# Kernel tuning notes

Hardware: AMD Instinct MI355X
Metric: run time of the kernel (lower is better)

## Reference

```python
import jax, jax.numpy as jnp
import numpy as np
import math

# static config
NH, HD, HID = 16, 128, 2048
ROT = 64            # head_dim * partial_rotary_factor(0.5)
EPS = 1e-6
GROUPS = 8
CHUNK = 64
THETA = 10000.0
LAYER_IDX, N_LAYERS = 1, 32
B, S = 2, 2048


def _base_slopes(n):
    # power-of-two branch of HF ALiBi slopes
    start = 2 ** (-(2 ** (-(math.log2(n) - 3))))
    return [start * (start ** i) for i in range(n)]

# per-head log-decay (negative): slope = -base * (1 - (l-1)/(L-1) + 1e-5)
SLOPE = jnp.asarray(
    -np.array(_base_slopes(NH), dtype=np.float32)
    * (1.0 - (LAYER_IDX - 1) / (N_LAYERS - 1) + 1e-5),
    dtype=jnp.float32)  # [NH]


def _rmsnorm(x, w):
    return x * jax.lax.rsqrt(jnp.mean(x * x, axis=-1, keepdims=True) + EPS) * w


def _partial_rope(x, positions):
    # x: [B,S,NH,HD]; neox-style rotary on first ROT dims, rest passthrough
    half = ROT // 2
    inv_freq = 1.0 / (THETA ** (jnp.arange(half, dtype=jnp.float32) / half))
    ang = positions.astype(jnp.float32)[:, None] * inv_freq       # [S, half]
    cos = jnp.cos(ang)[None, :, None, :]
    sin = jnp.sin(ang)[None, :, None, :]
    x1, x2, rest = x[..., :half], x[..., half:ROT], x[..., ROT:]
    return jnp.concatenate(
        [x1 * cos - x2 * sin, x2 * cos + x1 * sin, rest], axis=-1)


def setup_inputs() -> dict:
    key = jax.random.key(0)
    ks = jax.random.split(key, 4)
    return {
        'positions': jnp.arange(S, dtype=jnp.int32),
        'hidden_states': jax.random.normal(ks[0], (B, S, HID), jnp.float32),
        'recurrent_state': jnp.zeros((B, NH, HD, HD), jnp.float32),
        'w_qkv': jax.random.normal(ks[1], (HID, 3 * NH * HD), jnp.float32) * 0.02,
        'w_g': jax.random.normal(ks[2], (HID, NH * HD), jnp.float32) * 0.02,
        'w_dense': jax.random.normal(ks[3], (NH * HD, HID), jnp.float32) * 0.02,
        'q_norm_w': jnp.ones((HD,), jnp.float32),
        'k_norm_w': jnp.ones((HD,), jnp.float32),
        'g_norm_w': jnp.ones((NH * HD,), jnp.float32),
    }


def reference(positions, hidden_states, recurrent_state, w_qkv, w_g, w_dense,
              q_norm_w, k_norm_w, g_norm_w):
    # fused QKV projection
    qkv = hidden_states @ w_qkv                       # [B,S,3*NH*HD]
    q, k, v = jnp.split(qkv, 3, axis=-1)
    q = q.reshape(B, S, NH, HD)
    k = k.reshape(B, S, NH, HD)
    v = v.reshape(B, S, NH, HD)

    # QK RMSNorm then partial rotary
    q = _partial_rope(_rmsnorm(q, q_norm_w), positions)
    k = _partial_rope(_rmsnorm(k, k_norm_w), positions)

    # chunked ALiBi-decayed linear attention:
    #   S_t = lam * S_{t-1} + k_t v_t^T ; o_t = q_t S_t, lam = exp(slope)
    NC = S // CHUNK
    qc = q.reshape(B, NC, CHUNK, NH, HD).transpose(1, 0, 3, 2, 4)  # [NC,B,NH,C,HD]
    kc = k.reshape(B, NC, CHUNK, NH, HD).transpose(1, 0, 3, 2, 4)
    vc = v.reshape(B, NC, CHUNK, NH, HD).transpose(1, 0, 3, 2, 4)

    t = jnp.arange(CHUNK, dtype=jnp.float32)
    # intra-chunk causal decay mask lam^(i-j), i>=j: [NH,C,C]
    dec_mask = jnp.where(t[:, None] >= t[None, :],
                         jnp.exp(SLOPE[:, None, None] * (t[:, None] - t[None, :])),
                         0.0)
    q_dec = jnp.exp(SLOPE[:, None] * (t[None, :] + 1.0))            # [NH,C] lam^(i+1)
    k_dec = jnp.exp(SLOPE[:, None] * (CHUNK - 1.0 - t[None, :]))    # [NH,C] lam^(C-1-j)
    lam_C = jnp.exp(SLOPE * CHUNK)                                   # [NH]

    def step(state, inp):
        qb, kb, vb = inp                                  # [B,NH,C,HD]
        scores = jnp.einsum('bhid,bhjd->bhij', qb, kb) * dec_mask[None]
        o_intra = jnp.einsum('bhij,bhjd->bhid', scores, vb)
        o_inter = jnp.einsum('bhid,bhde->bhie', qb * q_dec[None, :, :, None], state)
        new_state = (state * lam_C[None, :, None, None]
                     + jnp.einsum('bhjd,bhje->bhde', kb * k_dec[None, :, :, None], vb))
        return new_state, o_intra + o_inter

    _, o = jax.lax.scan(step, recurrent_state, (qc, kc, vc))  # o: [NC,B,NH,C,HD]
    o = o.transpose(1, 0, 3, 2, 4).reshape(B, S, NH * HD)

    # GroupRMSNorm on attention output, sigmoid gate, output projection
    og = o.reshape(B, S, GROUPS, (NH * HD) // GROUPS)
    og = og * jax.lax.rsqrt(jnp.mean(og * og, axis=-1, keepdims=True) + EPS)
    o = og.reshape(B, S, NH * HD) * g_norm_w
    o = o * jax.nn.sigmoid(hidden_states @ w_g)
    return o @ w_dense
```

## Files before the change

kernel.cpp:

```cpp
#include <hip/hip_runtime.h>
#include <hip/hip_bf16.h>
#include <math.h>

#define NH   16
#define HD   128
#define HID  2048
#define NKV  6144
#define B_   2
#define S_   2048
#define NC   32
#define CHUNK_ 64
#define GROUPS_ 8

typedef __bf16 bf16_t;
typedef bf16_t bf16x8 __attribute__((ext_vector_type(8)));
typedef float  f32x4  __attribute__((ext_vector_type(4)));

__device__ __forceinline__ float b2f(unsigned int u) {
    union { unsigned int u; float f; } c; c.u = (u & 0xffffu) << 16; return c.f;
}
__device__ __forceinline__ unsigned int f2b(float f) {
    union { float f; unsigned int u; } c; c.f = f;
    unsigned int u = c.u;
    return (u + 0x7fffu + ((u >> 16) & 1u)) >> 16;
}

#define GLOAD_LDS16(gp, lp) __builtin_amdgcn_global_load_lds(                     \
    (const __attribute__((address_space(1))) void*)(gp),                          \
    (__attribute__((address_space(3))) void*)(lp), 16, 0, 0)

__global__ __launch_bounds__(256) void cvt_bf16(const float* __restrict__ in,
                                                unsigned short* __restrict__ out, int n8)
{
    int i = blockIdx.x * 256 + threadIdx.x;
    if (i >= n8) return;
    const float4* p = (const float4*)in + (size_t)i * 2;
    float4 a = p[0], b = p[1];
    uint4 o;
    o.x = f2b(a.x) | (f2b(a.y) << 16);
    o.y = f2b(a.z) | (f2b(a.w) << 16);
    o.z = f2b(b.x) | (f2b(b.y) << 16);
    o.w = f2b(b.z) | (f2b(b.w) << 16);
    ((uint4*)out)[i] = o;
}

__global__ __launch_bounds__(256) void transpose_cvt(const float* __restrict__ in,
                                                     unsigned short* __restrict__ out,
                                                     int Kdim, int Ndim)
{
    __shared__ float tile[32][33];
    int ntx = Ndim >> 5;
    int bx = blockIdx.x % ntx;
    int by = blockIdx.x / ntx;
    int lx = threadIdx.x & 31, ly = threadIdx.x >> 5;
    int r0 = by * 32, c0 = bx * 32;
    #pragma unroll
    for (int r = 0; r < 4; ++r)
        tile[ly + r * 8][lx] = in[(size_t)(r0 + ly + r * 8) * Ndim + c0 + lx];
    __syncthreads();
    #pragma unroll
    for (int r = 0; r < 4; ++r)
        out[(size_t)(c0 + ly + r * 8) * Kdim + r0 + lx] = (unsigned short)f2b(tile[lx][ly + r * 8]);
}

__device__ __forceinline__ void storeOne(float* p, float v) { *p = v; }
__device__ __forceinline__ void storeOne(unsigned short* p, float v) { *p = (unsigned short)f2b(v); }

template <typename OutT>
__global__ __launch_bounds__(256) void gemm_mfma(const bf16_t* __restrict__ A,
                                                 const bf16_t* __restrict__ Bt,
                                                 OutT* __restrict__ C,
                                                 int M, int N, int K)
{
    __shared__ bf16_t As[128 * 32];
    __shared__ bf16_t Bs[128 * 32];
    int tid  = threadIdx.x;
    int ntiles = N >> 7;
    int bx = blockIdx.x % ntiles;
    int by = blockIdx.x / ntiles;
    int lane = tid & 63;
    int wave = tid >> 6;
    int wm = (wave >> 1) * 64;
    int wn = (wave & 1) * 64;
    int l16  = lane & 15;
    int quad = lane >> 4;

    f32x4 acc[4][4];
    #pragma unroll
    for (int i = 0; i < 4; ++i)
        #pragma unroll
        for (int j = 0; j < 4; ++j) { f32x4 z = {0.f, 0.f, 0.f, 0.f}; acc[i][j] = z; }

    const bf16_t* aG = A  + (size_t)(by * 128 + (tid >> 2)) * K + (tid & 3) * 8;
    const bf16_t* bG = Bt + (size_t)(bx * 128 + (tid >> 2)) * K + (tid & 3) * 8;
    bf16_t* aL0 = As + tid * 8;
    bf16_t* aL1 = As + 2048 + tid * 8;
    bf16_t* bL0 = Bs + tid * 8;
    bf16_t* bL1 = Bs + 2048 + tid * 8;
    const size_t half = (size_t)64 * K;

    for (int kt = 0; kt < K; kt += 32) {
        GLOAD_LDS16(aG + kt,        aL0);
        GLOAD_LDS16(aG + half + kt, aL1);
        GLOAD_LDS16(bG + kt,        bL0);
        GLOAD_LDS16(bG + half + kt, bL1);
        __syncthreads();
        bf16x8 af[4], bf[4];
        #pragma unroll
        for (int t = 0; t < 4; ++t) {
            af[t] = *(const bf16x8*)(As + (wm + t * 16 + l16) * 32 + quad * 8);
            bf[t] = *(const bf16x8*)(Bs + (wn + t * 16 + l16) * 32 + quad * 8);
        }
        #pragma unroll
        for (int mt = 0; mt < 4; ++mt)
            #pragma unroll
            for (int nt = 0; nt < 4; ++nt)
                acc[mt][nt] = __builtin_amdgcn_mfma_f32_16x16x32_bf16(af[mt], bf[nt], acc[mt][nt], 0, 0, 0);
        __syncthreads();
    }

    #pragma unroll
    for (int mt = 0; mt < 4; ++mt)
        #pragma unroll
        for (int nt = 0; nt < 4; ++nt) {
            int col = bx * 128 + wn + nt * 16 + l16;
            #pragma unroll
            for (int r = 0; r < 4; ++r) {
                int row = by * 128 + wm + mt * 16 + quad * 4 + r;
                storeOne(C + (size_t)row * N + col, acc[mt][nt][r]);
            }
        }
}


__device__ __forceinline__ void ld_fr4(bf16x8 (&d)[4][2], const bf16_t* b, int s0, int ri) {
    #pragma unroll
    for (int i = 0; i < 4; ++i)
        #pragma unroll
        for (int k = 0; k < 2; ++k)
            d[i][k] = *(const bf16x8*)(b + (((s0 + i) * 2 + k) << 9) + ri);
}
__device__ __forceinline__ void ld_fr2(bf16x8 (&d)[2][2], const bf16_t* b, int s0, int ri) {
    #pragma unroll
    for (int i = 0; i < 2; ++i)
        #pragma unroll
        for (int k = 0; k < 2; ++k)
            d[i][k] = *(const bf16x8*)(b + (((s0 + i) * 2 + k) << 9) + ri);
}
__device__ __forceinline__ void mfma_quad(f32x4 (&a)[4][2], const bf16x8 (&af)[4][2],
                                          const bf16x8 (&bv)[2][2]) {
    #pragma unroll
    for (int mt = 0; mt < 4; ++mt)
        #pragma unroll
        for (int nt = 0; nt < 2; ++nt)
            #pragma unroll
            for (int ks = 0; ks < 2; ++ks)
                a[mt][nt] = __builtin_amdgcn_mfma_f32_16x16x32_bf16(af[mt][ks], bv[nt][ks], a[mt][nt], 0, 0, 0);
}

#define BAR()     asm volatile("s_barrier" ::: "memory")
#define VMCNT0()  asm volatile("s_waitcnt vmcnt(0)" ::: "memory")

__global__ __launch_bounds__(512, 2) void gemm_qg_256(const bf16_t* __restrict__ A,
                                                      const bf16_t* __restrict__ Bt,
                                                      unsigned short* __restrict__ Cq,
                                                      unsigned short* __restrict__ Cg)
{
    __shared__ bf16_t Asm[2][2][8192];
    __shared__ bf16_t Bsm[2][2][8192];
    const int K  = HID;
    const int NT = K / 64;

    int tid  = threadIdx.x;
    int wave = tid >> 6, lane = tid & 63;
    int wm = wave >> 2, wn = wave & 3;
    int l16 = lane & 15, quad = lane >> 4;
    int wm4 = wm * 4, wn2 = wn * 2;

    int bid = blockIdx.x;
    int xcd = bid & 7, idx = bid >> 3;
    int by  = (xcd >> 2) * 8 + (idx >> 3);
    int bx  = (xcd & 3) * 8 + (idx & 7);

    int rd_in = ((l16 << 5) | (quad << 3)) ^ (((l16 >> 3) & 1) << 4);

    int ch = lane ^ ((lane & 32) >> 4);
    int rr = ch >> 2;
    int cc = (ch & 3) * 8;

    const bf16_t* aSrc0 = A  + (size_t)(by * 256 +       wave * 16 + rr) * K + cc;
    const bf16_t* aSrc1 = A  + (size_t)(by * 256 + 128 + wave * 16 + rr) * K + cc;
    const bf16_t* bSrc0 = Bt + (size_t)(bx * 256 +       wave * 16 + rr) * K + cc;
    const bf16_t* bSrc1 = Bt + (size_t)(bx * 256 + 128 + wave * 16 + rr) * K + cc;

#define STAGE_A(h, t) do {                                                        \
        const bf16_t* _g = ((h) ? aSrc1 : aSrc0) + (size_t)(t) * 64;              \
        bf16_t* _l = &Asm[(t) & 1][(h)][wave * 1024 + lane * 8];                  \
        GLOAD_LDS16(_g,      _l);                                                 \
        GLOAD_LDS16(_g + 32, _l + 512); } while (0)
#define STAGE_B(h, t) do {                                                        \
        const bf16_t* _g = ((h) ? bSrc1 : bSrc0) + (size_t)(t) * 64;              \
        bf16_t* _l = &Bsm[(t) & 1][(h)][wave * 1024 + lane * 8];                  \
        GLOAD_LDS16(_g,      _l);                                                 \
        GLOAD_LDS16(_g + 32, _l + 512); } while (0)

    f32x4 acc[2][2][4][2];
    #pragma unroll
    for (int a0 = 0; a0 < 2; ++a0)
        #pragma unroll
        for (int a1 = 0; a1 < 2; ++a1)
            #pragma unroll
            for (int a2 = 0; a2 < 4; ++a2)
                #pragma unroll
                for (int a3 = 0; a3 < 2; ++a3) { f32x4 z = {0.f,0.f,0.f,0.f}; acc[a0][a1][a2][a3] = z; }

    STAGE_A(0, 0); STAGE_B(0, 0); STAGE_A(1, 0); STAGE_B(1, 0);
    VMCNT0();
    BAR();

    #pragma unroll 2
    for (int t = 0; t < NT - 1; ++t) {
        const int buf = t & 1;
        STAGE_A(0, t + 1); STAGE_B(0, t + 1); STAGE_A(1, t + 1); STAGE_B(1, t + 1);
        {
            bf16x8 afA[4][2], afB[4][2], bf0[2][2], bf1[2][2];
            ld_fr4(afA, &Asm[buf][0][0], wm4, rd_in);
            ld_fr2(bf0, &Bsm[buf][0][0], wn2, rd_in);
            mfma_quad(acc[0][0], afA, bf0);
            ld_fr2(bf1, &Bsm[buf][1][0], wn2, rd_in);
            mfma_quad(acc[0][1], afA, bf1);
            ld_fr4(afB, &Asm[buf][1][0], wm4, rd_in);
            mfma_quad(acc[1][1], afB, bf1);
            mfma_quad(acc[1][0], afB, bf0);
        }
        VMCNT0();
        BAR();
    }
    {
        const int buf = (NT - 1) & 1;
        bf16x8 afA[4][2], afB[4][2], bf0[2][2], bf1[2][2];
        ld_fr4(afA, &Asm[buf][0][0], wm4, rd_in);
        ld_fr2(bf0, &Bsm[buf][0][0], wn2, rd_in);
        mfma_quad(acc[0][0], afA, bf0);
        ld_fr2(bf1, &Bsm[buf][1][0], wn2, rd_in);
        mfma_quad(acc[0][1], afA, bf1);
        ld_fr4(afB, &Asm[buf][1][0], wm4, rd_in);
        mfma_quad(acc[1][1], afB, bf1);
        mfma_quad(acc[1][0], afB, bf0);
    }
#undef STAGE_A
#undef STAGE_B

    unsigned short* Cc; int Nn, colbase;
    if (bx < 24) { Cc = Cq; Nn = NKV; colbase = bx * 256; }
    else         { Cc = Cg; Nn = HID; colbase = bx * 256 - NKV; }
    int row0 = by * 256 + wm * 64 + quad * 4;
    int col0 = colbase + wn * 32 + l16;
    #pragma unroll
    for (int mh = 0; mh < 2; ++mh)
        #pragma unroll
        for (int nh = 0; nh < 2; ++nh)
            #pragma unroll
            for (int mt = 0; mt < 4; ++mt)
                #pragma unroll
                for (int nt = 0; nt < 2; ++nt) {
                    int col = col0 + nh * 128 + nt * 16;
                    #pragma unroll
                    for (int r = 0; r < 4; ++r) {
                        int row = row0 + mh * 128 + mt * 16 + r;
                        Cc[(size_t)row * Nn + col] = (unsigned short)f2b(acc[mh][nh][mt][nt][r]);
                    }
                }
}

__global__ __launch_bounds__(256) void norm_rope(unsigned short* __restrict__ qkv,
                                                 const int* __restrict__ positions,
                                                 const float* __restrict__ qw,
                                                 const float* __restrict__ kw)
{
    int bs = blockIdx.x;
    int s  = bs & (S_ - 1);
    int tid = threadIdx.x;
    int l16 = tid & 15;
    unsigned short* base = qkv + (size_t)bs * NKV;
    float pos = (float)positions[s];

    #pragma unroll
    for (int p = 0; p < 2; ++p) {
        int rr = p * 16 + (tid >> 4);
        int qk = rr >> 4;
        int h  = rr & 15;
        unsigned short* row = base + qk * HID + h * HD;
        const float* w = qk ? kw : qw;
        uint4 v = *(const uint4*)(row + l16 * 8);
        float x[8];
        x[0] = b2f(v.x); x[1] = b2f(v.x >> 16);
        x[2] = b2f(v.y); x[3] = b2f(v.y >> 16);
        x[4] = b2f(v.z); x[5] = b2f(v.z >> 16);
        x[6] = b2f(v.w); x[7] = b2f(v.w >> 16);
        float ss = 0.f;
        #pragma unroll
        for (int t = 0; t < 8; ++t) ss += x[t] * x[t];
        ss += __shfl_xor(ss, 1); ss += __shfl_xor(ss, 2);
        ss += __shfl_xor(ss, 4); ss += __shfl_xor(ss, 8);
        float inv = rsqrtf(ss * (1.0f / 128.0f) + 1e-6f);
        float n[8];
        #pragma unroll
        for (int t = 0; t < 8; ++t) n[t] = x[t] * inv * w[l16 * 8 + t];
        float pr[8];
        #pragma unroll
        for (int t = 0; t < 8; ++t) pr[t] = __shfl_xor(n[t], 4);
        if (l16 < 8) {
            #pragma unroll
            for (int t = 0; t < 8; ++t) {
                int dim = l16 * 8 + t;
                int i = dim & 31;
                float ang = pos * exp2f(-(float)i * 0.4152410118609203f);
                float cs = cosf(ang), sn = sinf(ang);
                n[t] = (dim < 32) ? (n[t] * cs - pr[t] * sn) : (n[t] * cs + pr[t] * sn);
            }
        }
        uint4 o;
        o.x = f2b(n[0]) | (f2b(n[1]) << 16);
        o.y = f2b(n[2]) | (f2b(n[3]) << 16);
        o.z = f2b(n[4]) | (f2b(n[5]) << 16);
        o.w = f2b(n[6]) | (f2b(n[7]) << 16);
        *(uint4*)(row + l16 * 8) = o;
    }
}

__global__ __launch_bounds__(256) void chunk_kv(const unsigned short* __restrict__ qkv,
                                                unsigned short* __restrict__ wbuf)
{
    __shared__ unsigned short kt[128 * 72];
    __shared__ unsigned short vt[128 * 72];
    int bi = blockIdx.x;
    int c = bi & 31, bh = bi >> 5, h = bh & 15, b = bh >> 4;
    int tid = threadIdx.x;
    float slope = -exp2f(-0.5f * (float)(h + 1)) * (1.0f + 1e-5f);

    const unsigned short* kbase = qkv + ((size_t)(b * S_ + c * CHUNK_)) * NKV + HID + h * HD;
    const unsigned short* vbase = kbase + HID;

    for (int idx = tid; idx < 4096; idx += 256) {
        int j = idx >> 6, p = idx & 63;
        unsigned int ku = *(const unsigned int*)(kbase + (size_t)j * NKV + p * 2);
        kt[(2 * p) * 72 + j]     = (unsigned short)(ku & 0xffffu);
        kt[(2 * p + 1) * 72 + j] = (unsigned short)(ku >> 16);
        float kd = expf(slope * (float)(63 - j));
        unsigned int vu = *(const unsigned int*)(vbase + (size_t)j * NKV + p * 2);
        vt[(2 * p) * 72 + j]     = (unsigned short)f2b(b2f(vu) * kd);
        vt[(2 * p + 1) * 72 + j] = (unsigned short)f2b(b2f(vu >> 16) * kd);
    }
    __syncthreads();

    int lane = tid & 63, wave = tid >> 6;
    int wm = (wave >> 1) * 64;
    int wn = (wave & 1) * 64;
    int l16 = lane & 15, quad = lane >> 4;

    f32x4 acc[4][4];
    #pragma unroll
    for (int i = 0; i < 4; ++i)
        #pragma unroll
        for (int j = 0; j < 4; ++j) { f32x4 z = {0.f,0.f,0.f,0.f}; acc[i][j] = z; }

    #pragma unroll
    for (int ks = 0; ks < 64; ks += 32) {
        bf16x8 af[4], bf[4];
        #pragma unroll
        for (int t = 0; t < 4; ++t) {
            af[t] = *(const bf16x8*)((const bf16_t*)vt + (wm + t * 16 + l16) * 72 + ks + quad * 8);
            bf[t] = *(const bf16x8*)((const bf16_t*)kt + (wn + t * 16 + l16) * 72 + ks + quad * 8);
        }
        #pragma unroll
        for (int mt = 0; mt < 4; ++mt)
            #pragma unroll
            for (int nt = 0; nt < 4; ++nt)
                acc[mt][nt] = __builtin_amdgcn_mfma_f32_16x16x32_bf16(af[mt], bf[nt], acc[mt][nt], 0, 0, 0);
    }

    unsigned short* wp = wbuf + ((size_t)bi << 14);
    #pragma unroll
    for (int mt = 0; mt < 4; ++mt)
        #pragma unroll
        for (int nt = 0; nt < 4; ++nt) {
            int dcol = wn + nt * 16 + l16;
            #pragma unroll
            for (int r = 0; r < 4; ++r) {
                int erow = wm + mt * 16 + quad * 4 + r;
                wp[(size_t)erow * 128 + dcol] = (unsigned short)f2b(acc[mt][nt][r]);
            }
        }
}

__global__ __launch_bounds__(256) void state_scan(const unsigned short* __restrict__ wbuf,
                                                  const float* __restrict__ rs0,
                                                  unsigned short* __restrict__ stbuf)
{
    int bi = blockIdx.x;
    int es = bi & 15, bh = bi >> 4, h = bh & 15, b = bh >> 4;
    int tid = threadIdx.x;
    float slope = -exp2f(-0.5f * (float)(h + 1)) * (1.0f + 1e-5f);
    float lam = expf(slope * 64.0f);

    int e  = es * 8 + (tid >> 5);
    int d0 = (tid & 31) * 4;

    float S[4];
    const float* rp = rs0 + ((size_t)(b * NH + h)) * HD * HD + e;
    #pragma unroll
    for (int t = 0; t < 4; ++t) S[t] = rp[(size_t)(d0 + t) * HD];

    size_t off = (size_t)e * 128 + d0;
    for (int c = 0; c < NC; ++c) {
        size_t base = (((size_t)bh * NC + c) << 14) + off;
        uint2 o;
        o.x = f2b(S[0]) | (f2b(S[1]) << 16);
        o.y = f2b(S[2]) | (f2b(S[3]) << 16);
        *(uint2*)(stbuf + base) = o;
        uint2 w = *(const uint2*)(wbuf + base);
        S[0] = S[0] * lam + b2f(w.x);
        S[1] = S[1] * lam + b2f(w.x >> 16);
        S[2] = S[2] * lam + b2f(w.y);
        S[3] = S[3] * lam + b2f(w.y >> 16);
    }
}

__global__ __launch_bounds__(256) void chunk_out(const unsigned short* __restrict__ qkv,
                                                 const unsigned short* __restrict__ stbuf,
                                                 unsigned short* __restrict__ obuf)
{
    __shared__ unsigned short qs[64 * 136];
    __shared__ unsigned short vt[128 * 72];
    __shared__ unsigned short sc[64 * 72];

    int bi = blockIdx.x;
    int c = bi & 31, bh = bi >> 5, h = bh & 15, b = bh >> 4;
    int tid = threadIdx.x;
    float slope = -exp2f(-0.5f * (float)(h + 1)) * (1.0f + 1e-5f);

    int lane = tid & 63, wave = tid >> 6;
    int l16 = lane & 15, quad = lane >> 4;
    int wn3 = wave * 32;

    const unsigned short* stp = stbuf + (((size_t)bh * NC + c) << 14);
    bf16x8 bsf[4][2];
    #pragma unroll
    for (int ksp4 = 0; ksp4 < 4; ++ksp4)
        #pragma unroll
        for (int nt = 0; nt < 2; ++nt)
            bsf[ksp4][nt] = *(const bf16x8*)((const bf16_t*)stp +
                (size_t)(wn3 + nt * 16 + l16) * 128 + ksp4 * 32 + quad * 8);

    const unsigned short* qrow = qkv + ((size_t)(b * S_ + c * CHUNK_)) * NKV + h * HD;
    const unsigned short* krow = qrow + HID;
    for (int idx = tid; idx < 1024; idx += 256) {
        int row = idx >> 4, c8 = (idx & 15) * 8;
        *(uint4*)(qs + row * 136 + c8) = *(const uint4*)(qrow + (size_t)row * NKV + c8);
    }
    const unsigned short* vbase = qrow + 2 * HID;
    for (int idx = tid; idx < 4096; idx += 256) {
        int j = idx >> 6, p = idx & 63;
        unsigned int vu = *(const unsigned int*)(vbase + (size_t)j * NKV + p * 2);
        vt[(2 * p) * 72 + j]     = (unsigned short)(vu & 0xffffu);
        vt[(2 * p + 1) * 72 + j] = (unsigned short)(vu >> 16);
    }
    __syncthreads();

    {
        f32x4 accS[4];
        #pragma unroll
        for (int t = 0; t < 4; ++t) { f32x4 z = {0.f,0.f,0.f,0.f}; accS[t] = z; }
        #pragma unroll
        for (int ksp = 0; ksp < 128; ksp += 32) {
            bf16x8 aq = *(const bf16x8*)((const bf16_t*)qs + (wave * 16 + l16) * 136 + ksp + quad * 8);
            #pragma unroll
            for (int nt = 0; nt < 4; ++nt) {
                bf16x8 bk = *(const bf16x8*)((const bf16_t*)krow + (size_t)(nt * 16 + l16) * NKV + ksp + quad * 8);
                accS[nt] = __builtin_amdgcn_mfma_f32_16x16x32_bf16(aq, bk, accS[nt], 0, 0, 0);
            }
        }
        float ad[4];
        #pragma unroll
        for (int r = 0; r < 4; ++r) ad[r] = expf(slope * (float)(wave * 16 + quad * 4 + r));
        #pragma unroll
        for (int nt = 0; nt < 4; ++nt) {
            int j = nt * 16 + l16;
            float bd = expf(-slope * (float)j);
            #pragma unroll
            for (int r = 0; r < 4; ++r) {
                int i = wave * 16 + quad * 4 + r;
                float v = (i >= j) ? accS[nt][r] * ad[r] * bd : 0.0f;
                sc[i * 72 + j] = (unsigned short)f2b(v);
            }
        }
    }
    __syncthreads();

    f32x4 accI[4][2], accE[4][2];
    #pragma unroll
    for (int i = 0; i < 4; ++i)
        #pragma unroll
        for (int j = 0; j < 2; ++j) { f32x4 z = {0.f,0.f,0.f,0.f}; accI[i][j] = z; accE[i][j] = z; }

    #pragma unroll
    for (int ksp = 0; ksp < 64; ksp += 32) {
        bf16x8 as[4], bv[2];
        #pragma unroll
        for (int mt = 0; mt < 4; ++mt)
            as[mt] = *(const bf16x8*)((const bf16_t*)sc + (mt * 16 + l16) * 72 + ksp + quad * 8);
        #pragma unroll
        for (int nt = 0; nt < 2; ++nt)
            bv[nt] = *(const bf16x8*)((const bf16_t*)vt + (wn3 + nt * 16 + l16) * 72 + ksp + quad * 8);
        #pragma unroll
        for (int mt = 0; mt < 4; ++mt)
            #pragma unroll
            for (int nt = 0; nt < 2; ++nt)
                accI[mt][nt] = __builtin_amdgcn_mfma_f32_16x16x32_bf16(as[mt], bv[nt], accI[mt][nt], 0, 0, 0);
    }
    #pragma unroll
    for (int ksp4 = 0; ksp4 < 4; ++ksp4) {
        bf16x8 aq[4];
        #pragma unroll
        for (int mt = 0; mt < 4; ++mt)
            aq[mt] = *(const bf16x8*)((const bf16_t*)qs + (mt * 16 + l16) * 136 + ksp4 * 32 + quad * 8);
        #pragma unroll
        for (int mt = 0; mt < 4; ++mt)
            #pragma unroll
            for (int nt = 0; nt < 2; ++nt)
                accE[mt][nt] = __builtin_amdgcn_mfma_f32_16x16x32_bf16(aq[mt], bsf[ksp4][nt], accE[mt][nt], 0, 0, 0);
    }

    #pragma unroll
    for (int mt = 0; mt < 4; ++mt) {
        #pragma unroll
        for (int r = 0; r < 4; ++r) {
            int i = mt * 16 + quad * 4 + r;
            float qd = expf(slope * (float)(i + 1));
            int orow = b * S_ + c * CHUNK_ + i;
            #pragma unroll
            for (int nt = 0; nt < 2; ++nt) {
                int col = h * HD + wn3 + nt * 16 + l16;
                float o = accI[mt][nt][r] + qd * accE[mt][nt][r];
                obuf[(size_t)orow * 2048 + col] = (unsigned short)f2b(o);
            }
        }
    }
}

__global__ __launch_bounds__(256) void gnorm_gate(const unsigned short* __restrict__ o,
                                                  unsigned short* __restrict__ gate,
                                                  const float* __restrict__ gw)
{
    int row = blockIdx.x >> 3;
    int g   = blockIdx.x & 7;
    int col = g * 256 + threadIdx.x;
    size_t idx = (size_t)row * 2048 + col;
    float ov = b2f(o[idx]);
    float ss = ov * ov;
    #pragma unroll
    for (int off = 32; off > 0; off >>= 1) ss += __shfl_xor(ss, off);
    __shared__ float part[4];
    if ((threadIdx.x & 63) == 0) part[threadIdx.x >> 6] = ss;
    __syncthreads();
    float tot = part[0] + part[1] + part[2] + part[3];
    float inv = rsqrtf(tot * (1.0f / 256.0f) + 1e-6f);
    float gv = b2f(gate[idx]);
    float sig = 1.0f / (1.0f + expf(-gv));
    gate[idx] = (unsigned short)f2b(ov * inv * gw[col] * sig);
}

extern "C" void kernel_launch(void* const* d_in, const int* in_sizes, int n_in,
                              void* d_out, int out_size, void* d_ws, size_t ws_size,
                              hipStream_t stream) {
    const int*   positions = (const int*)d_in[0];
    const float* hidden    = (const float*)d_in[1];
    const float* rstate    = (const float*)d_in[2];
    const float* w_qkv     = (const float*)d_in[3];
    const float* w_g       = (const float*)d_in[4];
    const float* w_dense   = (const float*)d_in[5];
    const float* q_norm_w  = (const float*)d_in[6];
    const float* k_norm_w  = (const float*)d_in[7];
    const float* g_norm_w  = (const float*)d_in[8];
    float* out = (float*)d_out;

    const int MR = B_ * S_;

    char* w = (char*)d_ws;
    unsigned short* qkv  = (unsigned short*)w;            w += (size_t)MR * NKV * 2;
    unsigned short* gbuf = (unsigned short*)w;            w += (size_t)MR * 2048 * 2;
    unsigned short* wdT  = (unsigned short*)w;            w += (size_t)HID * HID * 2;
    char* regionA = w;                                    w += (size_t)MR * HID * 2 + (size_t)8192 * HID * 2;
    char* regionB = w;
    unsigned short* hbf   = (unsigned short*)regionA;
    unsigned short* btQG  = (unsigned short*)(regionA + (size_t)MR * HID * 2);
    unsigned short* wqT   = btQG;
    unsigned short* wgT   = btQG + (size_t)NKV * HID;
    unsigned short* stbuf = (unsigned short*)regionA;
    unsigned short* wbuf  = (unsigned short*)regionB;
    unsigned short* obuf  = (unsigned short*)regionB;

    cvt_bf16<<<dim3((MR * HID / 8 + 255) / 256), dim3(256), 0, stream>>>(hidden, hbf, MR * HID / 8);
    transpose_cvt<<<dim3((HID / 32) * (NKV / 32)), dim3(256), 0, stream>>>(w_qkv, wqT, HID, NKV);
    transpose_cvt<<<dim3((HID / 32) * (HID / 32)), dim3(256), 0, stream>>>(w_g, wgT, HID, HID);
    transpose_cvt<<<dim3((HID / 32) * (HID / 32)), dim3(256), 0, stream>>>(w_dense, wdT, HID, HID);

    gemm_qg_256<<<dim3(512), dim3(512), 0, stream>>>(
        (const bf16_t*)hbf, (const bf16_t*)btQG, qkv, gbuf);
    norm_rope<<<dim3(B_ * S_), dim3(256), 0, stream>>>(qkv, positions, q_norm_w, k_norm_w);

    chunk_kv<<<dim3(B_ * NH * NC), dim3(256), 0, stream>>>(qkv, wbuf);
    state_scan<<<dim3(B_ * NH * 16), dim3(256), 0, stream>>>(wbuf, rstate, stbuf);
    chunk_out<<<dim3(B_ * NH * NC), dim3(256), 0, stream>>>(qkv, stbuf, obuf);

    gnorm_gate<<<dim3(MR * GROUPS_), dim3(256), 0, stream>>>(obuf, gbuf, g_norm_w);
    gemm_mfma<float><<<dim3((MR / 128) * (HID / 128)), dim3(256), 0, stream>>>(
        (const bf16_t*)gbuf, (const bf16_t*)wdT, out, MR, HID, HID);
}
```

Baseline: 459.0 us.

## Pre-pack B operand into MFMA fragment layout, add pipelined output GEMM

The weight transpose for the QKV/gate GEMM is replaced by a pack kernel that writes B directly in per-lane MFMA fragment order. The main GEMM then loads B fragments straight from global memory into registers with double buffering and drops the B LDS staging, halving LDS traffic and footprint. The output projection GEMM is replaced by a double-buffered, XCD-swizzled 128x128 kernel with swizzled LDS reads, and the state scan prefetches two chunks ahead. Register pressure rises, and the direct global B loads depend on L2 reuse across blocks.

```diff
diff --git a/kernel.cpp b/kernel.cpp
--- a/kernel.cpp
+++ b/kernel.cpp
@@ -63,73 +63,28 @@
         out[(size_t)(c0 + ly + r * 8) * Kdim + r0 + lx] = (unsigned short)f2b(tile[lx][ly + r * 8]);
 }
 
-__device__ __forceinline__ void storeOne(float* p, float v) { *p = v; }
-__device__ __forceinline__ void storeOne(unsigned short* p, float v) { *p = (unsigned short)f2b(v); }
-
-template <typename OutT>
-__global__ __launch_bounds__(256) void gemm_mfma(const bf16_t* __restrict__ A,
-                                                 const bf16_t* __restrict__ Bt,
-                                                 OutT* __restrict__ C,
-                                                 int M, int N, int K)
-{
-    __shared__ bf16_t As[128 * 32];
-    __shared__ bf16_t Bs[128 * 32];
-    int tid  = threadIdx.x;
-    int ntiles = N >> 7;
-    int bx = blockIdx.x % ntiles;
-    int by = blockIdx.x / ntiles;
-    int lane = tid & 63;
-    int wave = tid >> 6;
-    int wm = (wave >> 1) * 64;
-    int wn = (wave & 1) * 64;
-    int l16  = lane & 15;
-    int quad = lane >> 4;
-
-    f32x4 acc[4][4];
-    #pragma unroll
-    for (int i = 0; i < 4; ++i)
-        #pragma unroll
-        for (int j = 0; j < 4; ++j) { f32x4 z = {0.f, 0.f, 0.f, 0.f}; acc[i][j] = z; }
-
-    const bf16_t* aG = A  + (size_t)(by * 128 + (tid >> 2)) * K + (tid & 3) * 8;
-    const bf16_t* bG = Bt + (size_t)(bx * 128 + (tid >> 2)) * K + (tid & 3) * 8;
-    bf16_t* aL0 = As + tid * 8;
-    bf16_t* aL1 = As + 2048 + tid * 8;
-    bf16_t* bL0 = Bs + tid * 8;
-    bf16_t* bL1 = Bs + 2048 + tid * 8;
-    const size_t half = (size_t)64 * K;
-
-    for (int kt = 0; kt < K; kt += 32) {
-        GLOAD_LDS16(aG + kt,        aL0);
-        GLOAD_LDS16(aG + half + kt, aL1);
-        GLOAD_LDS16(bG + kt,        bL0);
-        GLOAD_LDS16(bG + half + kt, bL1);
-        __syncthreads();
-        bf16x8 af[4], bf[4];
-        #pragma unroll
-        for (int t = 0; t < 4; ++t) {
-            af[t] = *(const bf16x8*)(As + (wm + t * 16 + l16) * 32 + quad * 8);
-            bf[t] = *(const bf16x8*)(Bs + (wn + t * 16 + l16) * 32 + quad * 8);
-        }
-        #pragma unroll
-        for (int mt = 0; mt < 4; ++mt)
-            #pragma unroll
-            for (int nt = 0; nt < 4; ++nt)
-                acc[mt][nt] = __builtin_amdgcn_mfma_f32_16x16x32_bf16(af[mt], bf[nt], acc[mt][nt], 0, 0, 0);
-        __syncthreads();
-    }
-
-    #pragma unroll
-    for (int mt = 0; mt < 4; ++mt)
-        #pragma unroll
-        for (int nt = 0; nt < 4; ++nt) {
-            int col = bx * 128 + wn + nt * 16 + l16;
-            #pragma unroll
-            for (int r = 0; r < 4; ++r) {
-                int row = by * 128 + wm + mt * 16 + quad * 4 + r;
-                storeOne(C + (size_t)row * N + col, acc[mt][nt][r]);
-            }
-        }
+__global__ __launch_bounds__(256) void pack_b(const float* __restrict__ in,
+                                              unsigned short* __restrict__ out, int Ndim)
+{
+    __shared__ float tile[32][33];
+    int ntx = Ndim >> 5;
+    int bx = blockIdx.x % ntx;
+    int by = blockIdx.x / ntx;
+    int lx = threadIdx.x & 31, ly = threadIdx.x >> 5;
+    int r0 = by * 32, c0 = bx * 32;
+    #pragma unroll
+    for (int r = 0; r < 4; ++r)
+        tile[ly + r * 8][lx] = in[(size_t)(r0 + ly + r * 8) * Ndim + c0 + lx];
+    __syncthreads();
+    int quad = (lx >> 3) & 3;
+    int e    = lx & 7;
+    #pragma unroll
+    for (int r = 0; r < 4; ++r) {
+        int n = c0 + ly + r * 8;
+        int n16 = n >> 4, l16 = n & 15;
+        out[((size_t)(n16 * 64 + by) << 9) + (quad * 16 + l16) * 8 + e] =
+            (unsigned short)f2b(tile[lx][ly + r * 8]);
+    }
 }
 
 
@@ -140,13 +95,6 @@
         for (int k = 0; k < 2; ++k)
             d[i][k] = *(const bf16x8*)(b + (((s0 + i) * 2 + k) << 9) + ri);
 }
-__device__ __forceinline__ void ld_fr2(bf16x8 (&d)[2][2], const bf16_t* b, int s0, int ri) {
-    #pragma unroll
-    for (int i = 0; i < 2; ++i)
-        #pragma unroll
-        for (int k = 0; k < 2; ++k)
-            d[i][k] = *(const bf16x8*)(b + (((s0 + i) * 2 + k) << 9) + ri);
-}
 __device__ __forceinline__ void mfma_quad(f32x4 (&a)[4][2], const bf16x8 (&af)[4][2],
                                           const bf16x8 (&bv)[2][2]) {
     #pragma unroll
@@ -157,17 +105,27 @@
             for (int ks = 0; ks < 2; ++ks)
                 a[mt][nt] = __builtin_amdgcn_mfma_f32_16x16x32_bf16(af[mt][ks], bv[nt][ks], a[mt][nt], 0, 0, 0);
 }
+__device__ __forceinline__ void load_bfrag(bf16x8 (&d)[2][2][2], const bf16_t* Bp,
+                                           int n16b, int tt, int lane8) {
+    #pragma unroll
+    for (int nh = 0; nh < 2; ++nh)
+        #pragma unroll
+        for (int nt = 0; nt < 2; ++nt)
+            #pragma unroll
+            for (int ks = 0; ks < 2; ++ks)
+                d[nh][nt][ks] = *(const bf16x8*)(Bp +
+                    ((size_t)((n16b + nh * 8 + nt) * 64 + tt * 2 + ks) << 9) + lane8);
+}
 
 #define BAR()     asm volatile("s_barrier" ::: "memory")
 #define VMCNT0()  asm volatile("s_waitcnt vmcnt(0)" ::: "memory")
 
 __global__ __launch_bounds__(512, 2) void gemm_qg_256(const bf16_t* __restrict__ A,
-                                                      const bf16_t* __restrict__ Bt,
+                                                      const bf16_t* __restrict__ Bp,
                                                       unsigned short* __restrict__ Cq,
                                                       unsigned short* __restrict__ Cg)
 {
     __shared__ bf16_t Asm[2][2][8192];
-    __shared__ bf16_t Bsm[2][2][8192];
     const int K  = HID;
     const int NT = K / 64;
 
@@ -175,34 +133,30 @@
     int wave = tid >> 6, lane = tid & 63;
     int wm = wave >> 2, wn = wave & 3;
     int l16 = lane & 15, quad = lane >> 4;
-    int wm4 = wm * 4, wn2 = wn * 2;
+    int wm4 = wm * 4;
+    int lane8 = lane * 8;
 
     int bid = blockIdx.x;
     int xcd = bid & 7, idx = bid >> 3;
     int by  = (xcd >> 2) * 8 + (idx >> 3);
     int bx  = (xcd & 3) * 8 + (idx & 7);
 
+    int n16b = bx * 16 + wn * 2;
+
     int rd_in = ((l16 << 5) | (quad << 3)) ^ (((l16 >> 3) & 1) << 4);
 
     int ch = lane ^ ((lane & 32) >> 4);
     int rr = ch >> 2;
     int cc = (ch & 3) * 8;
 
-    const bf16_t* aSrc0 = A  + (size_t)(by * 256 +       wave * 16 + rr) * K + cc;
-    const bf16_t* aSrc1 = A  + (size_t)(by * 256 + 128 + wave * 16 + rr) * K + cc;
-    const bf16_t* bSrc0 = Bt + (size_t)(bx * 256 +       wave * 16 + rr) * K + cc;
-    const bf16_t* bSrc1 = Bt + (size_t)(bx * 256 + 128 + wave * 16 + rr) * K + cc;
+    const bf16_t* aSrc0 = A + (size_t)(by * 256 +       wave * 16 + rr) * K + cc;
+    const bf16_t* aSrc1 = A + (size_t)(by * 256 + 128 + wave * 16 + rr) * K + cc;
 
 #define STAGE_A(h, t) do {                                                        \
         const bf16_t* _g = ((h) ? aSrc1 : aSrc0) + (size_t)(t) * 64;              \
         bf16_t* _l = &Asm[(t) & 1][(h)][wave * 1024 + lane * 8];                  \
         GLOAD_LDS16(_g,      _l);                                                 \
         GLOAD_LDS16(_g + 32, _l + 512); } while (0)
-#define STAGE_B(h, t) do {                                                        \
-        const bf16_t* _g = ((h) ? bSrc1 : bSrc0) + (size_t)(t) * 64;              \
-        bf16_t* _l = &Bsm[(t) & 1][(h)][wave * 1024 + lane * 8];                  \
-        GLOAD_LDS16(_g,      _l);                                                 \
-        GLOAD_LDS16(_g + 32, _l + 512); } while (0)
 
     f32x4 acc[2][2][4][2];
     #pragma unroll
@@ -214,42 +168,42 @@
                 #pragma unroll
                 for (int a3 = 0; a3 < 2; ++a3) { f32x4 z = {0.f,0.f,0.f,0.f}; acc[a0][a1][a2][a3] = z; }
 
-    STAGE_A(0, 0); STAGE_B(0, 0); STAGE_A(1, 0); STAGE_B(1, 0);
+    bf16x8 af[4][2];
+    bf16x8 bfA[2][2][2], bfB[2][2][2];
+
+    load_bfrag(bfA, Bp, n16b, 0, lane8);
+    STAGE_A(0, 0); STAGE_A(1, 0);
     VMCNT0();
     BAR();
 
-    #pragma unroll 2
-    for (int t = 0; t < NT - 1; ++t) {
-        const int buf = t & 1;
-        STAGE_A(0, t + 1); STAGE_B(0, t + 1); STAGE_A(1, t + 1); STAGE_B(1, t + 1);
-        {
-            bf16x8 afA[4][2], afB[4][2], bf0[2][2], bf1[2][2];
-            ld_fr4(afA, &Asm[buf][0][0], wm4, rd_in);
-            ld_fr2(bf0, &Bsm[buf][0][0], wn2, rd_in);
-            mfma_quad(acc[0][0], afA, bf0);
-            ld_fr2(bf1, &Bsm[buf][1][0], wn2, rd_in);
-            mfma_quad(acc[0][1], afA, bf1);
-            ld_fr4(afB, &Asm[buf][1][0], wm4, rd_in);
-            mfma_quad(acc[1][1], afB, bf1);
-            mfma_quad(acc[1][0], afB, bf0);
-        }
-        VMCNT0();
-        BAR();
-    }
+#define QG_TILE(t, BFC, BFN) do {                                                 \
+        const int buf_ = (t) & 1;                                                 \
+        load_bfrag(BFN, Bp, n16b, (t) + 1, lane8);                                \
+        STAGE_A(0, (t) + 1); STAGE_A(1, (t) + 1);                                 \
+        ld_fr4(af, &Asm[buf_][0][0], wm4, rd_in);                                 \
+        mfma_quad(acc[0][0], af, BFC[0]);                                         \
+        mfma_quad(acc[0][1], af, BFC[1]);                                         \
+        ld_fr4(af, &Asm[buf_][1][0], wm4, rd_in);                                 \
+        mfma_quad(acc[1][1], af, BFC[1]);                                         \
+        mfma_quad(acc[1][0], af, BFC[0]);                                         \
+        VMCNT0();                                                                 \
+        BAR(); } while (0)
+
+    for (int t = 0; t < NT - 2; t += 2) {
+        QG_TILE(t,     bfA, bfB);
+        QG_TILE(t + 1, bfB, bfA);
+    }
+    QG_TILE(NT - 2, bfA, bfB);
     {
-        const int buf = (NT - 1) & 1;
-        bf16x8 afA[4][2], afB[4][2], bf0[2][2], bf1[2][2];
-        ld_fr4(afA, &Asm[buf][0][0], wm4, rd_in);
-        ld_fr2(bf0, &Bsm[buf][0][0], wn2, rd_in);
-        mfma_quad(acc[0][0], afA, bf0);
-        ld_fr2(bf1, &Bsm[buf][1][0], wn2, rd_in);
-        mfma_quad(acc[0][1], afA, bf1);
-        ld_fr4(afB, &Asm[buf][1][0], wm4, rd_in);
-        mfma_quad(acc[1][1], afB, bf1);
-        mfma_quad(acc[1][0], afB, bf0);
-    }
+        ld_fr4(af, &Asm[1][0][0], wm4, rd_in);
+        mfma_quad(acc[0][0], af, bfB[0]);
+        mfma_quad(acc[0][1], af, bfB[1]);
+        ld_fr4(af, &Asm[1][1][0], wm4, rd_in);
+        mfma_quad(acc[1][1], af, bfB[1]);
+        mfma_quad(acc[1][0], af, bfB[0]);
+    }
+#undef QG_TILE
 #undef STAGE_A
-#undef STAGE_B
 
     unsigned short* Cc; int Nn, colbase;
     if (bx < 24) { Cc = Cq; Nn = NKV; colbase = bx * 256; }
@@ -271,6 +225,91 @@
                         Cc[(size_t)row * Nn + col] = (unsigned short)f2b(acc[mh][nh][mt][nt][r]);
                     }
                 }
+}
+
+__global__ __launch_bounds__(256, 2) void gemm_out_128(const bf16_t* __restrict__ A,
+                                                       const bf16_t* __restrict__ Bt,
+                                                       float* __restrict__ C)
+{
+    __shared__ bf16_t As[2][4096];
+    __shared__ bf16_t Bs[2][4096];
+    const int K  = HID;
+    const int NT = K / 32;
+
+    int tid  = threadIdx.x;
+    int wave = tid >> 6, lane = tid & 63;
+    int wm2 = wave >> 1, wn2 = wave & 1;
+    int l16 = lane & 15, quad = lane >> 4;
+    int w2 = wave * 2;
+
+    int bid = blockIdx.x;
+    int xcd = bid & 7, idx = bid >> 3;
+    int by  = (xcd >> 1) * 8 + (idx >> 3);
+    int bx  = (xcd & 1) * 8 + (idx & 7);
+
+    int rd_in = ((l16 << 5) | (quad << 3)) ^ (((l16 >> 3) & 1) << 4);
+    int ch = lane ^ ((lane & 32) >> 4);
+    int rr = ch >> 2;
+    int cc = (ch & 3) * 8;
+
+    const bf16_t* aSrc = A  + (size_t)(by * 128 + w2 * 16 + rr) * K + cc;
+    const bf16_t* bSrc = Bt + (size_t)(bx * 128 + w2 * 16 + rr) * K + cc;
+
+#define OSTAGE(t) do {                                                            \
+        const int nb_ = (t) & 1;                                                  \
+        const bf16_t* _ga = aSrc + (size_t)(t) * 32;                              \
+        const bf16_t* _gb = bSrc + (size_t)(t) * 32;                              \
+        GLOAD_LDS16(_ga,                  &As[nb_][w2 * 512 + lane * 8]);         \
+        GLOAD_LDS16(_ga + (size_t)16 * K, &As[nb_][w2 * 512 + 512 + lane * 8]);   \
+        GLOAD_LDS16(_gb,                  &Bs[nb_][w2 * 512 + lane * 8]);         \
+        GLOAD_LDS16(_gb + (size_t)16 * K, &Bs[nb_][w2 * 512 + 512 + lane * 8]); } while (0)
+
+    f32x4 acc[4][4];
+    #pragma unroll
+    for (int i = 0; i < 4; ++i)
+        #pragma unroll
+        for (int j = 0; j < 4; ++j) { f32x4 z = {0.f,0.f,0.f,0.f}; acc[i][j] = z; }
+
+#define OCOMP(t) do {                                                             \
+        const int b_ = (t) & 1;                                                   \
+        bf16x8 af_[4], bf_[4];                                                    \
+        _Pragma("unroll")                                                         \
+        for (int i = 0; i < 4; ++i)                                               \
+            af_[i] = *(const bf16x8*)(&As[b_][((wm2 * 4 + i) << 9) + rd_in]);     \
+        _Pragma("unroll")                                                         \
+        for (int j = 0; j < 4; ++j)                                               \
+            bf_[j] = *(const bf16x8*)(&Bs[b_][((wn2 * 4 + j) << 9) + rd_in]);     \
+        _Pragma("unroll")                                                         \
+        for (int i = 0; i < 4; ++i)                                               \
+            _Pragma("unroll")                                                     \
+            for (int j = 0; j < 4; ++j)                                           \
+                acc[i][j] = __builtin_amdgcn_mfma_f32_16x16x32_bf16(af_[i], bf_[j], acc[i][j], 0, 0, 0); } while (0)
+
+    OSTAGE(0);
+    VMCNT0();
+    BAR();
+    #pragma unroll 2
+    for (int t = 0; t < NT - 1; ++t) {
+        OSTAGE(t + 1);
+        OCOMP(t);
+        VMCNT0();
+        BAR();
+    }
+    OCOMP(NT - 1);
+#undef OSTAGE
+#undef OCOMP
+
+    #pragma unroll
+    for (int i = 0; i < 4; ++i)
+        #pragma unroll
+        for (int j = 0; j < 4; ++j) {
+            int col = bx * 128 + wn2 * 64 + j * 16 + l16;
+            #pragma unroll
+            for (int r = 0; r < 4; ++r) {
+                int row = by * 128 + wm2 * 64 + i * 16 + quad * 4 + r;
+                C[(size_t)row * HID + col] = acc[i][j][r];
+            }
+        }
 }
 
 __global__ __launch_bounds__(256) void norm_rope(unsigned short* __restrict__ qkv,
@@ -413,17 +452,22 @@
     for (int t = 0; t < 4; ++t) S[t] = rp[(size_t)(d0 + t) * HD];
 
     size_t off = (size_t)e * 128 + d0;
+    size_t base = (((size_t)bh * NC) << 14) + off;
+    uint2 w0 = *(const uint2*)(wbuf + base);
+    uint2 w1 = *(const uint2*)(wbuf + base + (1 << 14));
     for (int c = 0; c < NC; ++c) {
-        size_t base = (((size_t)bh * NC + c) << 14) + off;
         uint2 o;
         o.x = f2b(S[0]) | (f2b(S[1]) << 16);
         o.y = f2b(S[2]) | (f2b(S[3]) << 16);
         *(uint2*)(stbuf + base) = o;
-        uint2 w = *(const uint2*)(wbuf + base);
-        S[0] = S[0] * lam + b2f(w.x);
-        S[1] = S[1] * lam + b2f(w.x >> 16);
-        S[2] = S[2] * lam + b2f(w.y);
-        S[3] = S[3] * lam + b2f(w.y >> 16);
+        uint2 w2 = w1;
+        if (c + 2 < NC) w2 = *(const uint2*)(wbuf + base + (2 << 14));
+        S[0] = S[0] * lam + b2f(w0.x);
+        S[1] = S[1] * lam + b2f(w0.x >> 16);
+        S[2] = S[2] * lam + b2f(w0.y);
+        S[3] = S[3] * lam + b2f(w0.y >> 16);
+        w0 = w1; w1 = w2;
+        base += (1 << 14);
     }
 }
 
@@ -594,20 +638,18 @@
     char* regionA = w;                                    w += (size_t)MR * HID * 2 + (size_t)8192 * HID * 2;
     char* regionB = w;
     unsigned short* hbf   = (unsigned short*)regionA;
-    unsigned short* btQG  = (unsigned short*)(regionA + (size_t)MR * HID * 2);
-    unsigned short* wqT   = btQG;
-    unsigned short* wgT   = btQG + (size_t)NKV * HID;
+    unsigned short* Bp    = (unsigned short*)(regionA + (size_t)MR * HID * 2);
     unsigned short* stbuf = (unsigned short*)regionA;
     unsigned short* wbuf  = (unsigned short*)regionB;
     unsigned short* obuf  = (unsigned short*)regionB;
 
     cvt_bf16<<<dim3((MR * HID / 8 + 255) / 256), dim3(256), 0, stream>>>(hidden, hbf, MR * HID / 8);
-    transpose_cvt<<<dim3((HID / 32) * (NKV / 32)), dim3(256), 0, stream>>>(w_qkv, wqT, HID, NKV);
-    transpose_cvt<<<dim3((HID / 32) * (HID / 32)), dim3(256), 0, stream>>>(w_g, wgT, HID, HID);
+    pack_b<<<dim3((HID / 32) * (NKV / 32)), dim3(256), 0, stream>>>(w_qkv, Bp, NKV);
+    pack_b<<<dim3((HID / 32) * (HID / 32)), dim3(256), 0, stream>>>(w_g, Bp + (size_t)384 * 64 * 512, HID);
     transpose_cvt<<<dim3((HID / 32) * (HID / 32)), dim3(256), 0, stream>>>(w_dense, wdT, HID, HID);
 
     gemm_qg_256<<<dim3(512), dim3(512), 0, stream>>>(
-        (const bf16_t*)hbf, (const bf16_t*)btQG, qkv, gbuf);
+        (const bf16_t*)hbf, (const bf16_t*)Bp, qkv, gbuf);
     norm_rope<<<dim3(B_ * S_), dim3(256), 0, stream>>>(qkv, positions, q_norm_w, k_norm_w);
 
     chunk_kv<<<dim3(B_ * NH * NC), dim3(256), 0, stream>>>(qkv, wbuf);
@@ -615,6 +657,6 @@
     chunk_out<<<dim3(B_ * NH * NC), dim3(256), 0, stream>>>(qkv, stbuf, obuf);
 
     gnorm_gate<<<dim3(MR * GROUPS_), dim3(256), 0, stream>>>(obuf, gbuf, g_norm_w);
-    gemm_mfma<float><<<dim3((MR / 128) * (HID / 128)), dim3(256), 0, stream>>>(
-        (const bf16_t*)gbuf, (const bf16_t*)wdT, out, MR, HID, HID);
-}
+    gemm_out_128<<<dim3(512), dim3(256), 0, stream>>>(
+        (const bf16_t*)gbuf, (const bf16_t*)wdT, out);
+}
```

Measured after the change: 436.5 us. -4.9%, faster.
